# Performance work log

Hardware: AMD Instinct MI355X
Metric: run time of the kernel (lower is better)

The kernel has to match this reference:

```python
import jax, jax.numpy as jnp
import numpy as np

B, S, D, H, E = 2, 2048, 1024, 2048, 8


def setup_inputs() -> dict:
    key = jax.random.key(0)
    ks = jax.random.split(key, 5)
    scale_in = 0.02
    x = jax.random.normal(ks[0], (B, S, D), dtype=jnp.float32)
    Wr = jax.random.normal(ks[1], (D, E), dtype=jnp.float32) * scale_in
    br = jnp.zeros((E,), dtype=jnp.float32)
    W1 = jax.random.normal(ks[2], (E, D, H), dtype=jnp.float32) * (1.0 / np.sqrt(D))
    b1 = jnp.zeros((E, H), dtype=jnp.float32)
    W2 = jax.random.normal(ks[3], (E, H, D), dtype=jnp.float32) * (1.0 / np.sqrt(H))
    b2 = jnp.zeros((E, D), dtype=jnp.float32)
    return {"x": x, "Wr": Wr, "br": br, "W1": W1, "b1": b1, "W2": W2, "b2": b2, "k": 2}


def reference(x, Wr, br, W1, b1, W2, b2, k):
    # Router: top-k logits, softmax over the k selected logits
    logits = x @ Wr + br                       # [B,S,E]
    top_v, top_i = jax.lax.top_k(logits, k)    # [B,S,k]
    scores = jax.nn.softmax(top_v, axis=-1)    # [B,S,k]

    # Dense all-expert MLP (reference combine): [B,S,E,*]
    h = jax.nn.relu(jnp.einsum('bsd,edh->bseh', x, W1) + b1[None, None])
    eo = jnp.einsum('bseh,ehd->bsed', h, W2) + b2[None, None]  # [B,S,E,D]

    # Gather the k selected experts per token and combine with scores
    sel = jnp.take_along_axis(eo, top_i[..., None], axis=2)   # [B,S,k,D]
    out = jnp.sum(scores[..., None] * sel, axis=2)             # [B,S,D]
    return out
```

## Files before the change

kernel.cpp:

```cpp
#include <hip/hip_runtime.h>
#include <hip/hip_bf16.h>

#define TOKENS 4096
#define DDIM 1024
#define HDIM 2048
#define NEXP 8
#define NASSIGN 8192
#define MAX_TILES 80

typedef __attribute__((ext_vector_type(8))) __bf16 bf16x8;
typedef __attribute__((ext_vector_type(4))) float f32x4;
typedef __attribute__((ext_vector_type(4))) unsigned short u16x4;

__device__ __forceinline__ unsigned short f2bf(float f) {
    unsigned int u = __builtin_bit_cast(unsigned int, f);
    u += 0x7fffu + ((u >> 16) & 1u);
    return (unsigned short)(u >> 16);
}

__global__ __launch_bounds__(256) void router_kernel(
    const float* __restrict__ x, const float* __restrict__ Wr, const float* __restrict__ br,
    unsigned short* __restrict__ x_bf, int* __restrict__ topk_e, float* __restrict__ topk_s)
{
    const int t = blockIdx.x * 4 + (threadIdx.x >> 6);
    const int lane = threadIdx.x & 63;
    const float* xr = x + (long)t * DDIM;
    unsigned short* xo = x_bf + (long)t * DDIM;
    float acc[8] = {0.f,0.f,0.f,0.f,0.f,0.f,0.f,0.f};
    for (int it = 0; it < DDIM / 64; ++it) {
        const int d = it * 64 + lane;
        const float xv = xr[d];
        xo[d] = f2bf(xv);
        const float4 w0 = *(const float4*)(Wr + d * 8);
        const float4 w1 = *(const float4*)(Wr + d * 8 + 4);
        acc[0] += xv * w0.x; acc[1] += xv * w0.y; acc[2] += xv * w0.z; acc[3] += xv * w0.w;
        acc[4] += xv * w1.x; acc[5] += xv * w1.y; acc[6] += xv * w1.z; acc[7] += xv * w1.w;
    }
#pragma unroll
    for (int e = 0; e < 8; ++e) {
        float v = acc[e];
        for (int off = 32; off > 0; off >>= 1) v += __shfl_down(v, off, 64);
        acc[e] = v;
    }
    if (lane == 0) {
        float lg[8];
#pragma unroll
        for (int e = 0; e < 8; ++e) lg[e] = acc[e] + br[e];
        int i0 = 0; float v0 = lg[0];
#pragma unroll
        for (int e = 1; e < 8; ++e) if (lg[e] > v0) { v0 = lg[e]; i0 = e; }
        int i1 = -1; float v1 = -3.4e38f;
#pragma unroll
        for (int e = 0; e < 8; ++e) if (e != i0 && lg[e] > v1) { v1 = lg[e]; i1 = e; }
        const float e1 = expf(v1 - v0);
        const float inv = 1.f / (1.f + e1);
        topk_e[t * 2]     = i0; topk_s[t * 2]     = inv;
        topk_e[t * 2 + 1] = i1; topk_s[t * 2 + 1] = e1 * inv;
    }
}

__global__ __launch_bounds__(1024) void build_lists_kernel(
    const int* __restrict__ topk_e, const float* __restrict__ topk_s,
    int* __restrict__ token_list, float* __restrict__ score_list, int* __restrict__ meta)
{
    __shared__ int cnt[NEXP];
    __shared__ int base[NEXP];
    __shared__ int cur[NEXP];
    const int tid = threadIdx.x;
    if (tid < NEXP) cnt[tid] = 0;
    __syncthreads();
    for (int i = tid; i < NASSIGN; i += 1024) atomicAdd(&cnt[topk_e[i]], 1);
    __syncthreads();
    if (tid == 0) {
        int accu = 0;
        for (int e = 0; e < NEXP; ++e) { base[e] = accu; cur[e] = accu; accu += cnt[e]; }
        int ntile = 0;
        for (int e = 0; e < NEXP; ++e) {
            const int c = cnt[e];
            for (int r = 0; r * 128 < c; ++r) {
                meta[1 + ntile] = e;
                meta[1 + MAX_TILES + ntile] = base[e] + r * 128;
                meta[1 + 2 * MAX_TILES + ntile] = (c - r * 128) < 128 ? (c - r * 128) : 128;
                ++ntile;
            }
        }
        meta[0] = ntile;
    }
    __syncthreads();
    for (int i = tid; i < NASSIGN; i += 1024) {
        const int e = topk_e[i];
        const int slot = atomicAdd(&cur[e], 1);
        token_list[slot] = i >> 1;
        score_list[slot] = topk_s[i];
    }
}

__global__ __launch_bounds__(256) void transpose_cvt_kernel(
    const float* __restrict__ W1, const float* __restrict__ W2,
    unsigned short* __restrict__ W1t, unsigned short* __restrict__ W2t)
{
    __shared__ unsigned short tile[64 * 68];
    const int z = blockIdx.y;
    const bool is1 = z < 8;
    const int e = is1 ? z : z - 8;
    const int K = is1 ? DDIM : HDIM;
    const int N = is1 ? HDIM : DDIM;
    const float* src = (is1 ? W1 : W2) + (long)e * K * N;
    unsigned short* dst = (is1 ? W1t : W2t) + (long)e * K * N;
    const int ktiles = K >> 6;
    const int k0 = (blockIdx.x % ktiles) * 64;
    const int n0 = (blockIdx.x / ktiles) * 64;
    const int r0 = threadIdx.x >> 4;
    const int c4 = (threadIdx.x & 15) * 4;
#pragma unroll
    for (int i = 0; i < 4; ++i) {
        const int r = r0 + i * 16;
        const float4 v = *(const float4*)(src + (long)(k0 + r) * N + n0 + c4);
        tile[(c4 + 0) * 68 + r] = f2bf(v.x);
        tile[(c4 + 1) * 68 + r] = f2bf(v.y);
        tile[(c4 + 2) * 68 + r] = f2bf(v.z);
        tile[(c4 + 3) * 68 + r] = f2bf(v.w);
    }
    __syncthreads();
#pragma unroll
    for (int i = 0; i < 4; ++i) {
        const int rn = r0 + i * 16;
        u16x4 o;
        o.x = tile[rn * 68 + c4 + 0];
        o.y = tile[rn * 68 + c4 + 1];
        o.z = tile[rn * 68 + c4 + 2];
        o.w = tile[rn * 68 + c4 + 3];
        *(u16x4*)(dst + (long)(n0 + rn) * K + k0 + c4) = o;
    }
}

template<int KDIM, int NDIM, bool G2>
__global__ __launch_bounds__(256, 2) void expert_gemm(
    const unsigned short* __restrict__ Abase,
    const unsigned short* __restrict__ Bt,
    const float* __restrict__ bias,
    unsigned short* __restrict__ Hout,
    float* __restrict__ Out,
    const int* __restrict__ token_list,
    const float* __restrict__ score_list,
    const int* __restrict__ meta)
{
    const int nt = meta[0];
    const int xcd = blockIdx.x & 7;
    const int off = blockIdx.x >> 3;
    const int q = nt >> 3;
    const int r = nt & 7;
    const int cnt_i = q + (xcd < r ? 1 : 0);
    if (off >= cnt_i) return;
    const int t = xcd * q + (xcd < r ? xcd : r) + off;
    const int e = meta[1 + t];
    const int slot0 = meta[1 + MAX_TILES + t];
    const int rows_valid = meta[1 + 2 * MAX_TILES + t];
    const int n0 = blockIdx.y * 128;

    __shared__ unsigned short As[128 * 64];
    __shared__ unsigned short Bs[128 * 64];

    const int tid = threadIdx.x;
    const int lane = tid & 63;
    const int w = tid >> 6;
    const int wm = w & 1;
    const int wn = w >> 1;
    const int quad = lane >> 4;
    const int l15 = lane & 15;

    const unsigned short* aptr[4];
    const unsigned short* bptr[4];
    unsigned short* lA[4];
    unsigned short* lB[4];
#pragma unroll
    for (int c = 0; c < 4; ++c) {
        const int chunk = c * 256 + tid;
        const int row = chunk >> 3;
        const int kc = (chunk & 7) ^ (row & 7);
        const int rr = row < rows_valid ? row : rows_valid - 1;
        const long arow = G2 ? (long)(slot0 + rr) : (long)token_list[slot0 + rr];
        aptr[c] = Abase + arow * (long)KDIM + kc * 8;
        bptr[c] = Bt + ((long)e * NDIM + n0 + row) * (long)KDIM + kc * 8;
        lA[c] = &As[(c * 256 + w * 64) * 8];
        lB[c] = &Bs[(c * 256 + w * 64) * 8];
    }

    f32x4 acc[4][4] = {};

#pragma unroll 1
    for (int k0 = 0; k0 < KDIM; k0 += 64) {
#pragma unroll
        for (int c = 0; c < 4; ++c) {
            __builtin_amdgcn_global_load_lds(
                (const __attribute__((address_space(1))) unsigned int*)aptr[c],
                (__attribute__((address_space(3))) unsigned int*)lA[c], 16, 0, 0);
            aptr[c] += 64;
        }
#pragma unroll
        for (int c = 0; c < 4; ++c) {
            __builtin_amdgcn_global_load_lds(
                (const __attribute__((address_space(1))) unsigned int*)bptr[c],
                (__attribute__((address_space(3))) unsigned int*)lB[c], 16, 0, 0);
            bptr[c] += 64;
        }
        __syncthreads();

#pragma unroll
        for (int h = 0; h < 2; ++h) {
            bf16x8 af[4], bfr[4];
#pragma unroll
            for (int mi = 0; mi < 4; ++mi)
                af[mi] = *(const bf16x8*)&As[(wm * 64 + mi * 16 + l15) * 64 + ((h * 4 + quad) ^ (l15 & 7)) * 8];
#pragma unroll
            for (int ni = 0; ni < 4; ++ni)
                bfr[ni] = *(const bf16x8*)&Bs[(wn * 64 + ni * 16 + l15) * 64 + ((h * 4 + quad) ^ (l15 & 7)) * 8];
#pragma unroll
            for (int mi = 0; mi < 4; ++mi)
#pragma unroll
                for (int ni = 0; ni < 4; ++ni)
                    acc[mi][ni] = __builtin_amdgcn_mfma_f32_16x16x32_bf16(af[mi], bfr[ni], acc[mi][ni], 0, 0, 0);
        }
        __syncthreads();
    }

#pragma unroll
    for (int mi = 0; mi < 4; ++mi) {
#pragma unroll
        for (int ni = 0; ni < 4; ++ni) {
            const int col = n0 + wn * 64 + ni * 16 + l15;
#pragma unroll
            for (int rr = 0; rr < 4; ++rr) {
                const int row = wm * 64 + mi * 16 + quad * 4 + rr;
                if (row < rows_valid) {
                    float v = acc[mi][ni][rr] + bias[e * NDIM + col];
                    if (!G2) {
                        v = v > 0.f ? v : 0.f;
                        Hout[(long)(slot0 + row) * NDIM + col] = f2bf(v);
                    } else {
                        const int slot = slot0 + row;
                        const int tok = token_list[slot];
                        const float s = score_list[slot];
                        unsafeAtomicAdd(&Out[(long)tok * NDIM + col], s * v);
                    }
                }
            }
        }
    }
}

extern "C" void kernel_launch(void* const* d_in, const int* in_sizes, int n_in,
                              void* d_out, int out_size, void* d_ws, size_t ws_size,
                              hipStream_t stream)
{
    (void)in_sizes; (void)n_in; (void)out_size; (void)ws_size;
    const float* x  = (const float*)d_in[0];
    const float* Wr = (const float*)d_in[1];
    const float* br = (const float*)d_in[2];
    const float* W1 = (const float*)d_in[3];
    const float* b1 = (const float*)d_in[4];
    const float* W2 = (const float*)d_in[5];
    const float* b2 = (const float*)d_in[6];
    float* out = (float*)d_out;

    char* ws = (char*)d_ws;
    unsigned short* x_bf  = (unsigned short*)(ws);
    unsigned short* W1t   = (unsigned short*)(ws + 8388608);
    unsigned short* W2t   = (unsigned short*)(ws + 41943040);
    unsigned short* hbuf  = (unsigned short*)(ws + 75497472);
    int*   topk_e     = (int*)(ws + 109051904);
    float* topk_s     = (float*)(ws + 109084672);
    int*   token_list = (int*)(ws + 109117440);
    float* score_list = (float*)(ws + 109150208);
    int*   meta       = (int*)(ws + 109182976);

    hipMemsetAsync(d_out, 0, (size_t)TOKENS * DDIM * sizeof(float), stream);

    router_kernel<<<TOKENS / 4, 256, 0, stream>>>(x, Wr, br, x_bf, topk_e, topk_s);
    build_lists_kernel<<<1, 1024, 0, stream>>>(topk_e, topk_s, token_list, score_list, meta);
    transpose_cvt_kernel<<<dim3(512, 16), 256, 0, stream>>>(W1, W2, W1t, W2t);
    expert_gemm<DDIM, HDIM, false><<<dim3(MAX_TILES, HDIM / 128), 256, 0, stream>>>(
        x_bf, W1t, b1, hbuf, nullptr, token_list, score_list, meta);
    expert_gemm<HDIM, DDIM, true><<<dim3(MAX_TILES, DDIM / 128), 256, 0, stream>>>(
        hbuf, W2t, b2, nullptr, out, token_list, score_list, meta);
}
```

Measured before the change: 337.5 us.

## Double-buffer LDS tiles with BK=32 to overlap global loads with MFMA

Replaces the single-buffered BK=64 shared tiles with two BK=32 buffers and a software pipeline. The next k-slice is prefetched with global_load_lds while the current one is computed, and sync uses manual s_waitcnt vmcnt(4) plus s_barrier instead of __syncthreads. The XOR swizzle is reworked for the 32-wide row layout. This is meant to hide global memory latency behind the MFMA work, at the cost of twice as many loop iterations and barriers and reliance on hand-written waitcnt correctness.

```diff
diff --git a/kernel.cpp b/kernel.cpp
--- a/kernel.cpp
+++ b/kernel.cpp
@@ -158,8 +158,8 @@
     const int rows_valid = meta[1 + 2 * MAX_TILES + t];
     const int n0 = blockIdx.y * 128;
 
-    __shared__ unsigned short As[128 * 64];
-    __shared__ unsigned short Bs[128 * 64];
+    __shared__ unsigned short As[2][128 * 32];
+    __shared__ unsigned short Bs[2][128 * 32];
 
     const int tid = threadIdx.x;
     const int lane = tid & 63;
@@ -169,60 +169,65 @@
     const int quad = lane >> 4;
     const int l15 = lane & 15;
 
-    const unsigned short* aptr[4];
-    const unsigned short* bptr[4];
-    unsigned short* lA[4];
-    unsigned short* lB[4];
-#pragma unroll
-    for (int c = 0; c < 4; ++c) {
+    const unsigned short* aptr[2];
+    const unsigned short* bptr[2];
+    int ldsoff[2];
+#pragma unroll
+    for (int c = 0; c < 2; ++c) {
         const int chunk = c * 256 + tid;
-        const int row = chunk >> 3;
-        const int kc = (chunk & 7) ^ (row & 7);
+        const int row = chunk >> 2;
+        const int kc = (chunk & 3) ^ ((row >> 1) & 3);
         const int rr = row < rows_valid ? row : rows_valid - 1;
         const long arow = G2 ? (long)(slot0 + rr) : (long)token_list[slot0 + rr];
         aptr[c] = Abase + arow * (long)KDIM + kc * 8;
         bptr[c] = Bt + ((long)e * NDIM + n0 + row) * (long)KDIM + kc * 8;
-        lA[c] = &As[(c * 256 + w * 64) * 8];
-        lB[c] = &Bs[(c * 256 + w * 64) * 8];
+        ldsoff[c] = (c * 256 + w * 64) * 8;
     }
 
     f32x4 acc[4][4] = {};
-
+    constexpr int NITER = KDIM / 32;
+
+    auto issue = [&](int buf, int kof) {
+#pragma unroll
+        for (int c = 0; c < 2; ++c)
+            __builtin_amdgcn_global_load_lds(
+                (const __attribute__((address_space(1))) unsigned int*)(aptr[c] + kof),
+                (__attribute__((address_space(3))) unsigned int*)&As[buf][ldsoff[c]], 16, 0, 0);
+#pragma unroll
+        for (int c = 0; c < 2; ++c)
+            __builtin_amdgcn_global_load_lds(
+                (const __attribute__((address_space(1))) unsigned int*)(bptr[c] + kof),
+                (__attribute__((address_space(3))) unsigned int*)&Bs[buf][ldsoff[c]], 16, 0, 0);
+    };
+
+    auto compute = [&](int buf) {
+        const unsigned short* Ab = As[buf];
+        const unsigned short* Bb = Bs[buf];
+        const int slot = (quad ^ ((l15 >> 1) & 3)) * 8;
+        bf16x8 af[4], bfr[4];
+#pragma unroll
+        for (int mi = 0; mi < 4; ++mi)
+            af[mi] = *(const bf16x8*)&Ab[(wm * 64 + mi * 16 + l15) * 32 + slot];
+#pragma unroll
+        for (int ni = 0; ni < 4; ++ni)
+            bfr[ni] = *(const bf16x8*)&Bb[(wn * 64 + ni * 16 + l15) * 32 + slot];
+#pragma unroll
+        for (int mi = 0; mi < 4; ++mi)
+#pragma unroll
+            for (int ni = 0; ni < 4; ++ni)
+                acc[mi][ni] = __builtin_amdgcn_mfma_f32_16x16x32_bf16(af[mi], bfr[ni], acc[mi][ni], 0, 0, 0);
+    };
+
+    issue(0, 0);
 #pragma unroll 1
-    for (int k0 = 0; k0 < KDIM; k0 += 64) {
-#pragma unroll
-        for (int c = 0; c < 4; ++c) {
-            __builtin_amdgcn_global_load_lds(
-                (const __attribute__((address_space(1))) unsigned int*)aptr[c],
-                (__attribute__((address_space(3))) unsigned int*)lA[c], 16, 0, 0);
-            aptr[c] += 64;
-        }
-#pragma unroll
-        for (int c = 0; c < 4; ++c) {
-            __builtin_amdgcn_global_load_lds(
-                (const __attribute__((address_space(1))) unsigned int*)bptr[c],
-                (__attribute__((address_space(3))) unsigned int*)lB[c], 16, 0, 0);
-            bptr[c] += 64;
-        }
-        __syncthreads();
-
-#pragma unroll
-        for (int h = 0; h < 2; ++h) {
-            bf16x8 af[4], bfr[4];
-#pragma unroll
-            for (int mi = 0; mi < 4; ++mi)
-                af[mi] = *(const bf16x8*)&As[(wm * 64 + mi * 16 + l15) * 64 + ((h * 4 + quad) ^ (l15 & 7)) * 8];
-#pragma unroll
-            for (int ni = 0; ni < 4; ++ni)
-                bfr[ni] = *(const bf16x8*)&Bs[(wn * 64 + ni * 16 + l15) * 64 + ((h * 4 + quad) ^ (l15 & 7)) * 8];
-#pragma unroll
-            for (int mi = 0; mi < 4; ++mi)
-#pragma unroll
-                for (int ni = 0; ni < 4; ++ni)
-                    acc[mi][ni] = __builtin_amdgcn_mfma_f32_16x16x32_bf16(af[mi], bfr[ni], acc[mi][ni], 0, 0, 0);
-        }
-        __syncthreads();
-    }
+    for (int k = 0; k < NITER - 1; ++k) {
+        issue((k + 1) & 1, (k + 1) * 32);
+        asm volatile("s_waitcnt vmcnt(4)\n\ts_barrier" ::: "memory");
+        compute(k & 1);
+        asm volatile("s_barrier" ::: "memory");
+    }
+    asm volatile("s_waitcnt vmcnt(0)\n\ts_barrier" ::: "memory");
+    compute((NITER - 1) & 1);
 
 #pragma unroll
     for (int mi = 0; mi < 4; ++mi) {
```

New measurement: 353.3 us. 4.7% more time.
